# Kernel tuning notes

Measured on AMD Instinct MI355X. Metric: run time of the kernel, lower is better.

## Reference

```python
import jax, jax.numpy as jnp
import numpy as np

B, T, D, H = 512, 256, 64, 256


def setup_inputs() -> dict:
    key = jax.random.key(0)
    ks = jax.random.split(key, 12)
    X = jax.random.normal(ks[0], (B, T, D), dtype=jnp.float32)
    M = (jax.random.uniform(ks[1], (B, T, D)) < 0.7).astype(jnp.float32)
    # time since last observation, hours
    Delta = jax.random.uniform(ks[2], (B, T, D), dtype=jnp.float32) * 5.0
    x_mean = jax.random.normal(ks[3], (D,), dtype=jnp.float32) * 0.1
    s = 1.0 / np.sqrt(D)
    sh = 1.0 / np.sqrt(H)
    # input-decay Linear(D->D), hidden-decay Linear(D->H)
    W_gx = jax.random.uniform(ks[4], (D, D), minval=-s, maxval=s, dtype=jnp.float32)
    b_gx = jnp.zeros((D,), jnp.float32)
    W_gh = jax.random.uniform(ks[5], (D, H), minval=-s, maxval=s, dtype=jnp.float32)
    b_gh = jnp.zeros((H,), jnp.float32)
    # stacked gate weights for [z, r, h_tilde]
    W_x = jax.random.uniform(ks[6], (3, D, H), minval=-s, maxval=s, dtype=jnp.float32)
    W_h = jax.random.uniform(ks[7], (3, H, H), minval=-sh, maxval=sh, dtype=jnp.float32)
    W_m = jax.random.uniform(ks[8], (3, D, H), minval=-s, maxval=s, dtype=jnp.float32)
    b_g = jnp.zeros((3, H), jnp.float32)
    W_cls = jax.random.uniform(ks[9], (H, 1), minval=-sh, maxval=sh, dtype=jnp.float32)
    b_cls = jnp.zeros((1,), jnp.float32)
    return dict(X=X, M=M, Delta=Delta, x_mean=x_mean,
                W_gx=W_gx, b_gx=b_gx, W_gh=W_gh, b_gh=b_gh,
                W_x=W_x, W_h=W_h, W_m=W_m, b_g=b_g,
                W_cls=W_cls, b_cls=b_cls)


def reference(X, M, Delta, x_mean, W_gx, b_gx, W_gh, b_gh,
              W_x, W_h, W_m, b_g, W_cls, b_cls):
    Bn, Tn, Dn = X.shape
    Hn = W_h.shape[-1]

    def step(carry, inp):
        h, x_prev = carry          # [B,H], [B,D]
        x, m, d = inp              # each [B,D]
        gamma_x = jnp.exp(-jax.nn.relu(d @ W_gx + b_gx))   # [B,D]
        gamma_h = jnp.exp(-jax.nn.relu(d @ W_gh + b_gh))   # [B,H]
        # mean imputation with input decay
        x_hat = m * x + (1.0 - m) * (gamma_x * x_prev + (1.0 - gamma_x) * x_mean)
        hd = gamma_h * h                                   # hidden decay
        z = jax.nn.sigmoid(x_hat @ W_x[0] + hd @ W_h[0] + m @ W_m[0] + b_g[0])
        r = jax.nn.sigmoid(x_hat @ W_x[1] + hd @ W_h[1] + m @ W_m[1] + b_g[1])
        h_tilde = jnp.tanh(x_hat @ W_x[2] + (r * hd) @ W_h[2] + m @ W_m[2] + b_g[2])
        h_new = (1.0 - z) * hd + z * h_tilde
        x_prev_new = m * x + (1.0 - m) * x_prev            # carry last observation
        return (h_new, x_prev_new), None

    h0 = jnp.zeros((Bn, Hn), X.dtype)
    xp0 = jnp.zeros((Bn, Dn), X.dtype)
    xs = (jnp.swapaxes(X, 0, 1), jnp.swapaxes(M, 0, 1), jnp.swapaxes(Delta, 0, 1))
    (h, _), _ = jax.lax.scan(step, (h0, xp0), xs)
    return (h @ W_cls + b_cls)[:, 0]   # [B], classifier(h).squeeze(-1)
```

## Files before the change

kernel.cpp:

```cpp
#include <hip/hip_runtime.h>


constexpr int Bn = 512, Tn = 256, Dn = 64, Hn = 256;
constexpr int BB = 16, NBLK = Bn / BB;
constexpr int TC = 128;

typedef __attribute__((ext_vector_type(8))) short bf8_t;
typedef __attribute__((ext_vector_type(4))) float f4_t;

constexpr size_t OFF_WH  = 0;
constexpr size_t OFF_WX  = 196608;
constexpr size_t OFF_WM  = 245760;
constexpr size_t OFF_WGH = 294912;
constexpr size_t OFF_WGX = 311296;
constexpr int    PACK_SLOTS = 39424;

constexpr size_t GX_OFF  = (size_t)1 << 20;
constexpr size_t GH_OFF  = GX_OFF + (size_t)Bn * Tn * Dn * 4;
constexpr size_t WS_NEED = GH_OFF + (size_t)Bn * Tn * Hn * 2;

constexpr size_t GH2_OFF = (size_t)1 << 20;
constexpr size_t GX2_OFF = GH2_OFF + (size_t)Bn * Tn * Hn * 2;
constexpr size_t P2_OFF  = GX2_OFF;
constexpr size_t P2_SZ   = (size_t)3 * Bn * TC * Hn * 2;
constexpr size_t XH2_OFF = P2_OFF + P2_SZ;
constexpr size_t HST_OFF = XH2_OFF + (size_t)Bn * Tn * Dn * 2;
constexpr size_t WS_NEED3 = HST_OFF + (size_t)Bn * Hn * 2;

__device__ __forceinline__ unsigned short f2bf(float x) {
    union { float f; unsigned int u; } v; v.f = x;
    unsigned int r = (v.u + 0x7fffu + ((v.u >> 16) & 1u)) >> 16;
    return (unsigned short)r;
}
__device__ __forceinline__ float bf2f(unsigned short u) {
    union { unsigned int i; float f; } v; v.i = ((unsigned int)u) << 16; return v.f;
}
__device__ __forceinline__ bf8_t LD8(const short* p) { return *(const bf8_t*)p; }
__device__ __forceinline__ f4_t MF(bf8_t a, bf8_t b, f4_t c) {
    return __builtin_amdgcn_mfma_f32_16x16x32_bf16(a, b, c, 0, 0, 0);
}
__device__ __forceinline__ f4_t MFp(bf8_t a, const short* bp, f4_t c) {
    return MF(a, LD8(bp), c);
}
__device__ __forceinline__ const short* BA(const short* p, int ntG, int KT, int kt, int lane) {
    return p + (((size_t)ntG * KT + kt) * 64 + lane) * 8;
}
__device__ __forceinline__ void lds_sync() {
    __builtin_amdgcn_sched_barrier(0);
    asm volatile("s_waitcnt lgkmcnt(0)" ::: "memory");
    __builtin_amdgcn_s_barrier();
    __builtin_amdgcn_sched_barrier(0);
}

__global__ __launch_bounds__(256) void pack_weights(
    const float* __restrict__ W_gx, const float* __restrict__ W_gh,
    const float* __restrict__ W_x,  const float* __restrict__ W_h,
    const float* __restrict__ W_m,  short* __restrict__ out)
{
    const int slot = blockIdx.x * 256 + threadIdx.x;
    if (slot >= PACK_SLOTS) return;

    const float* w; int ldn, l, kt, j, kbase;
    if (slot < 24576) {
        int g = slot >> 13, rem = slot & 8191;
        int ntG = rem >> 9, r2 = rem & 511;
        kt = r2 >> 6; l = r2 & 63;
        j = ntG * 16 + (l & 15);
        w = W_h + (size_t)g * Hn * Hn; ldn = Hn;
    } else if (slot < 30720) {
        int s = slot - 24576;
        int g = s >> 11, rem = s & 2047;
        int ntG = rem >> 7, r2 = rem & 127;
        kt = r2 >> 6; l = r2 & 63;
        j = ntG * 16 + (l & 15);
        w = W_x + (size_t)g * Dn * Hn; ldn = Hn;
    } else if (slot < 36864) {
        int s = slot - 30720;
        int g = s >> 11, rem = s & 2047;
        int ntG = rem >> 7, r2 = rem & 127;
        kt = r2 >> 6; l = r2 & 63;
        j = ntG * 16 + (l & 15);
        w = W_m + (size_t)g * Dn * Hn; ldn = Hn;
    } else if (slot < 38912) {
        int s = slot - 36864;
        int ntG = s >> 7, r2 = s & 127;
        kt = r2 >> 6; l = r2 & 63;
        j = ntG * 16 + (l & 15);
        w = W_gh; ldn = Hn;
    } else {
        int s = slot - 38912;
        int ntG = s >> 7, r2 = s & 127;
        kt = r2 >> 6; l = r2 & 63;
        j = ntG * 16 + (l & 15);
        w = W_gx; ldn = Dn;
    }
    kbase = kt * 32 + ((l >> 4) << 3);
    bf8_t v;
    #pragma unroll
    for (int i = 0; i < 8; ++i)
        v[i] = (short)f2bf(w[(size_t)(kbase + i) * ldn + j]);
    *(bf8_t*)&out[(size_t)slot * 8] = v;
}

__global__ __launch_bounds__(256) void grud_prepass(
    const float* __restrict__ Dl, const float* __restrict__ b_gx,
    const float* __restrict__ b_gh, const short* __restrict__ pk,
    float* __restrict__ gx, unsigned short* __restrict__ gh)
{
    __shared__ short sDf[2 * 64 * 8];
    const int tid = threadIdx.x, w = tid >> 6, lane = tid & 63;
    const int bt = blockIdx.x >> 8, t = blockIdx.x & 255;
    const int b0 = bt * 16;
    const int c15 = lane & 15, rowb = (lane >> 4) * 4;

    if (w < 2) {
        const int row = lane & 15, cb = w * 32 + ((lane >> 4) << 3);
        const float* p = Dl + ((size_t)(b0 + row) * Tn + t) * Dn + cb;
        float4 a = *(const float4*)p, b = *(const float4*)(p + 4);
        bf8_t v;
        v[0]=(short)f2bf(a.x); v[1]=(short)f2bf(a.y); v[2]=(short)f2bf(a.z); v[3]=(short)f2bf(a.w);
        v[4]=(short)f2bf(b.x); v[5]=(short)f2bf(b.y); v[6]=(short)f2bf(b.z); v[7]=(short)f2bf(b.w);
        *(bf8_t*)&sDf[(w * 64 + lane) * 8] = v;
    }
    __syncthreads();
    bf8_t df0 = *(const bf8_t*)&sDf[lane * 8];
    bf8_t df1 = *(const bf8_t*)&sDf[(64 + lane) * 8];

    #pragma unroll
    for (int i = 0; i < 4; ++i) {
        const int ntG = 4 * w + i;
        f4_t acc = {0.f, 0.f, 0.f, 0.f};
        acc = MFp(df0, BA(pk + OFF_WGH, ntG, 2, 0, lane), acc);
        acc = MFp(df1, BA(pk + OFF_WGH, ntG, 2, 1, lane), acc);
        const int col = ntG * 16 + c15;
        const float bb = b_gh[col];
        #pragma unroll
        for (int q = 0; q < 4; ++q) {
            const int r = rowb + q;
            gh[((size_t)(b0 + r) * Tn + t) * Hn + col] =
                f2bf(__expf(-fmaxf(acc[q] + bb, 0.f)));
        }
    }
    {
        f4_t acc = {0.f, 0.f, 0.f, 0.f};
        acc = MFp(df0, BA(pk + OFF_WGX, w, 2, 0, lane), acc);
        acc = MFp(df1, BA(pk + OFF_WGX, w, 2, 1, lane), acc);
        const int col = w * 16 + c15;
        const float bb = b_gx[col];
        #pragma unroll
        for (int q = 0; q < 4; ++q) {
            const int r = rowb + q;
            gx[((size_t)(b0 + r) * Tn + t) * Dn + col] =
                __expf(-fmaxf(acc[q] + bb, 0.f));
        }
    }
}

__global__ __launch_bounds__(256) void grud_xhat(
    const float* __restrict__ X, const float* __restrict__ M,
    const float* __restrict__ x_mean, const float* __restrict__ gx,
    unsigned short* __restrict__ XH)
{
    const int g = blockIdx.x * 256 + threadIdx.x;
    const int b = g >> 6, d = g & 63;
    const float xm = x_mean[d];
    float xp = 0.f;
    const size_t base = (size_t)b * Tn * Dn + d;
    for (int t = 0; t < Tn; ++t) {
        const size_t idx = base + (size_t)t * Dn;
        const float x = X[idx], m = M[idx], gv = gx[idx];
        const float xh = m * x + (1.f - m) * (gv * xp + (1.f - gv) * xm);
        xp = m * x + (1.f - m) * xp;
        XH[idx] = f2bf(xh);
    }
}

__global__ __launch_bounds__(256) void grud_pgemm_c(
    const float* __restrict__ M, const unsigned short* __restrict__ XH,
    const float* __restrict__ b_g, const short* __restrict__ pk,
    unsigned short* __restrict__ P, int t0)
{
    const int tid = threadIdx.x, w = tid >> 6, lane = tid & 63;
    const int c15 = lane & 15;
    const int bblk = blockIdx.x >> 7;
    const int tl = blockIdx.x & (TC - 1);
    const int b0 = bblk * 16, t = t0 + tl;

    const size_t abase = ((size_t)(b0 + (lane & 15)) * Tn + t) * Dn + ((lane >> 4) << 3);
    bf8_t xf[2], mf[2];
    #pragma unroll
    for (int kt = 0; kt < 2; ++kt) {
        uint4 xa = *(const uint4*)&XH[abase + kt * 32];
        union { uint4 u; bf8_t b; } cvt; cvt.u = xa;
        xf[kt] = cvt.b;
        float4 a = *(const float4*)&M[abase + kt * 32];
        float4 b = *(const float4*)&M[abase + kt * 32 + 4];
        bf8_t v;
        v[0]=(short)f2bf(a.x); v[1]=(short)f2bf(a.y); v[2]=(short)f2bf(a.z); v[3]=(short)f2bf(a.w);
        v[4]=(short)f2bf(b.x); v[5]=(short)f2bf(b.y); v[6]=(short)f2bf(b.z); v[7]=(short)f2bf(b.w);
        mf[kt] = v;
    }

    const size_t btl = (size_t)blockIdx.x;
    #pragma unroll
    for (int i = 0; i < 12; ++i) {
        const int p = w * 12 + i;
        const int gg = p >> 4, ntG = p & 15;
        f4_t acc = {0.f, 0.f, 0.f, 0.f};
        acc = MFp(xf[0], BA(pk + OFF_WX + (size_t)gg * 16384, ntG, 2, 0, lane), acc);
        acc = MFp(xf[1], BA(pk + OFF_WX + (size_t)gg * 16384, ntG, 2, 1, lane), acc);
        acc = MFp(mf[0], BA(pk + OFF_WM + (size_t)gg * 16384, ntG, 2, 0, lane), acc);
        acc = MFp(mf[1], BA(pk + OFF_WM + (size_t)gg * 16384, ntG, 2, 1, lane), acc);
        const float bb = b_g[gg * Hn + ntG * 16 + c15];
        ushort4 o;
        o.x = f2bf(acc[0] + bb); o.y = f2bf(acc[1] + bb);
        o.z = f2bf(acc[2] + bb); o.w = f2bf(acc[3] + bb);
        *(ushort4*)&P[((btl * 3 + gg) * 16 + ntG) * 256 + lane * 4] = o;
    }
}

__global__ __launch_bounds__(512, 2) void grud_rec13(
    const float* __restrict__ W_cls, const float* __restrict__ b_cls,
    const short* __restrict__ pk, const unsigned short* __restrict__ gh,
    const unsigned short* __restrict__ P, unsigned short* __restrict__ hst,
    float* __restrict__ out, int t0, int lastc)
{
    __shared__ short sWh1[16 * 8 * 64 * 8];
    __shared__ unsigned short sh_hb[16][264];
    __shared__ short sA_hd[8 * 64 * 8];
    __shared__ short sA_rhd[8 * 64 * 8];

    const int tid = threadIdx.x, w = tid >> 6, lane = tid & 63;
    const int c15 = lane & 15, rowb = (lane >> 4) * 4;
    const int b0 = blockIdx.x * BB;
    unsigned short* hs = hst + (size_t)blockIdx.x * 16 * Hn;

    bf8_t whz[2][8], whh[2][8];
    #pragma unroll
    for (int nt = 0; nt < 2; ++nt)
        #pragma unroll
        for (int kt = 0; kt < 8; ++kt) {
            whz[nt][kt] = LD8(BA(pk + OFF_WH,             2 * w + nt, 8, kt, lane));
            whh[nt][kt] = LD8(BA(pk + OFF_WH + 2 * 65536, 2 * w + nt, 8, kt, lane));
        }
    for (int c = tid; c < 8192; c += 512)
        *(uint4*)&sWh1[c * 8] = *(const uint4*)&pk[OFF_WH + 65536 + (size_t)c * 8];

    float h_cd[2][4];
    if (t0 == 0) {
        for (int i = tid; i < 16 * 264; i += 512) (&sh_hb[0][0])[i] = 0;
        #pragma unroll
        for (int nt = 0; nt < 2; ++nt)
            #pragma unroll
            for (int q = 0; q < 4; ++q) h_cd[nt][q] = 0.f;
    } else {
        for (int i = tid; i < 16 * 256; i += 512)
            sh_hb[i >> 8][i & 255] = hs[i];
        #pragma unroll
        for (int nt = 0; nt < 2; ++nt)
            #pragma unroll
            for (int q = 0; q < 4; ++q)
                h_cd[nt][q] = bf2f(hs[(rowb + q) * Hn + w * 32 + nt * 16 + c15]);
    }

    const size_t ghA_base = ((size_t)(b0 + (lane & 15)) * Tn) * Hn + w * 32 + ((lane >> 4) << 3);
    uint4 gha = *(const uint4*)&gh[ghA_base + (size_t)t0 * Hn];
    unsigned short ghcd[2][4];
    #pragma unroll
    for (int nt = 0; nt < 2; ++nt)
        #pragma unroll
        for (int q = 0; q < 4; ++q)
            ghcd[nt][q] = gh[((size_t)(b0 + rowb + q) * Tn + t0) * Hn + w * 32 + nt * 16 + c15];

    ushort4 pz[2], pr[2], ph[2];
    {
        const size_t pbl = (size_t)blockIdx.x * TC;
        #pragma unroll
        for (int nt = 0; nt < 2; ++nt) {
            pz[nt] = *(const ushort4*)&P[((pbl * 3 + 0) * 16 + 2 * w + nt) * 256 + lane * 4];
            pr[nt] = *(const ushort4*)&P[((pbl * 3 + 1) * 16 + 2 * w + nt) * 256 + lane * 4];
            ph[nt] = *(const ushort4*)&P[((pbl * 3 + 2) * 16 + 2 * w + nt) * 256 + lane * 4];
        }
    }
    float hd_cd[2][4], zz[2][4];
    const f4_t z4 = {0.f, 0.f, 0.f, 0.f};
    __syncthreads();

    for (int tl = 0; tl < TC; ++tl) {
        const int tnl = (tl + 1 < TC) ? (tl + 1) : (TC - 1);
        const int tn  = t0 + tnl;

        {
            uint4 hA = *(const uint4*)&sh_hb[lane & 15][w * 32 + ((lane >> 4) << 3)];
            unsigned int ga[4] = {gha.x, gha.y, gha.z, gha.w};
            unsigned int ha[4] = {hA.x, hA.y, hA.z, hA.w};
            bf8_t hv;
            #pragma unroll
            for (int i = 0; i < 8; ++i) {
                float gf = bf2f((unsigned short)((ga[i >> 1] >> ((i & 1) * 16)) & 0xffffu));
                float hf = bf2f((unsigned short)((ha[i >> 1] >> ((i & 1) * 16)) & 0xffffu));
                hv[i] = (short)f2bf(gf * hf);
            }
            *(bf8_t*)&sA_hd[(w * 64 + lane) * 8] = hv;
        }
        #pragma unroll
        for (int nt = 0; nt < 2; ++nt)
            #pragma unroll
            for (int q = 0; q < 4; ++q)
                hd_cd[nt][q] = bf2f(ghcd[nt][q]) * h_cd[nt][q];

        uint4 gha_n = *(const uint4*)&gh[ghA_base + (size_t)tn * Hn];
        unsigned short ghcd_n[2][4];
        #pragma unroll
        for (int nt = 0; nt < 2; ++nt)
            #pragma unroll
            for (int q = 0; q < 4; ++q)
                ghcd_n[nt][q] = gh[((size_t)(b0 + rowb + q) * Tn + tn) * Hn + w * 32 + nt * 16 + c15];
        ushort4 pz_n[2], pr_n[2], ph_n[2];
        {
            const size_t pbl = (size_t)blockIdx.x * TC + tnl;
            #pragma unroll
            for (int nt = 0; nt < 2; ++nt) {
                pz_n[nt] = *(const ushort4*)&P[((pbl * 3 + 0) * 16 + 2 * w + nt) * 256 + lane * 4];
                pr_n[nt] = *(const ushort4*)&P[((pbl * 3 + 1) * 16 + 2 * w + nt) * 256 + lane * 4];
                ph_n[nt] = *(const ushort4*)&P[((pbl * 3 + 2) * 16 + 2 * w + nt) * 256 + lane * 4];
            }
        }
        lds_sync();

        f4_t aZ[2] = {z4, z4}, aR[2] = {z4, z4};
        #pragma unroll
        for (int kt = 0; kt < 8; ++kt) {
            bf8_t hf  = LD8(&sA_hd[(kt * 64 + lane) * 8]);
            bf8_t wr0 = LD8(&sWh1[((2 * w + 0) * 8 + kt) * 512 + lane * 8]);
            bf8_t wr1 = LD8(&sWh1[((2 * w + 1) * 8 + kt) * 512 + lane * 8]);
            aZ[0] = MF(hf, whz[0][kt], aZ[0]);
            aZ[1] = MF(hf, whz[1][kt], aZ[1]);
            aR[0] = MF(hf, wr0, aR[0]);
            aR[1] = MF(hf, wr1, aR[1]);
        }
        #pragma unroll
        for (int nt = 0; nt < 2; ++nt) {
            const int col = w * 32 + nt * 16 + c15;
            #pragma unroll
            for (int q = 0; q < 4; ++q) {
                const int r = rowb + q;
                float z  = 1.f / (1.f + __expf(-(aZ[nt][q] + bf2f(((const unsigned short*)&pz[nt])[q]))));
                float rr = 1.f / (1.f + __expf(-(aR[nt][q] + bf2f(((const unsigned short*)&pr[nt])[q]))));
                zz[nt][q] = z;
                sA_rhd[(w * 64 + ((col & 31) >> 3) * 16 + r) * 8 + (col & 7)] =
                    (short)f2bf(rr * hd_cd[nt][q]);
            }
        }
        lds_sync();

        f4_t aH[2] = {z4, z4};
        #pragma unroll
        for (int kt = 0; kt < 8; ++kt) {
            bf8_t rf = LD8(&sA_rhd[(kt * 64 + lane) * 8]);
            aH[0] = MF(rf, whh[0][kt], aH[0]);
            aH[1] = MF(rf, whh[1][kt], aH[1]);
        }
        #pragma unroll
        for (int nt = 0; nt < 2; ++nt) {
            const int col = w * 32 + nt * 16 + c15;
            #pragma unroll
            for (int q = 0; q < 4; ++q) {
                const int r = rowb + q;
                float pre = aH[nt][q] + bf2f(((const unsigned short*)&ph[nt])[q]);
                float a = fabsf(pre), e = __expf(-2.f * a);
                float th = copysignf((1.f - e) / (1.f + e), pre);
                float hn = (1.f - zz[nt][q]) * hd_cd[nt][q] + zz[nt][q] * th;
                h_cd[nt][q] = hn;
                sh_hb[r][col] = f2bf(hn);
            }
        }
        lds_sync();

        gha = gha_n;
        #pragma unroll
        for (int nt = 0; nt < 2; ++nt) {
            #pragma unroll
            for (int q = 0; q < 4; ++q) ghcd[nt][q] = ghcd_n[nt][q];
            pz[nt] = pz_n[nt]; pr[nt] = pr_n[nt]; ph[nt] = ph_n[nt];
        }
    }

    if (!lastc) {
        for (int i = tid; i < 16 * 256; i += 512)
            hs[i] = sh_hb[i >> 8][i & 255];
    } else {
        #pragma unroll
        for (int rr2 = 0; rr2 < 2; ++rr2) {
            const int row = w * 2 + rr2;
            ushort4 hb = *(const ushort4*)&sh_hb[row][lane * 4];
            float4 wv  = *(const float4*)&W_cls[lane * 4];
            float p = bf2f(hb.x) * wv.x + bf2f(hb.y) * wv.y +
                      bf2f(hb.z) * wv.z + bf2f(hb.w) * wv.w;
            #pragma unroll
            for (int o = 32; o > 0; o >>= 1) p += __shfl_down(p, o, 64);
            if (lane == 0) out[b0 + row] = p + b_cls[0];
        }
    }
}

__global__ __launch_bounds__(512, 2) void grud_rec8(
    const float* __restrict__ X, const float* __restrict__ M,
    const float* __restrict__ x_mean, const float* __restrict__ b_g,
    const float* __restrict__ W_cls, const float* __restrict__ b_cls,
    const short* __restrict__ pk, const float* __restrict__ gx,
    const unsigned short* __restrict__ gh, float* __restrict__ out)
{
    __shared__ short sWh1[16 * 8 * 64 * 8];
    __shared__ unsigned short sh_hb[16][264];
    __shared__ short sA_xh[2 * 64 * 8];
    __shared__ short sA_m [2 * 64 * 8];
    __shared__ short sA_hd[8 * 64 * 8];
    __shared__ short sA_rhd[8 * 64 * 8];

    const int tid = threadIdx.x, w = tid >> 6, lane = tid & 63;
    const int c15 = lane & 15, rowb = (lane >> 4) * 4;
    const int b0 = blockIdx.x * BB;

    bf8_t whz[2][8], whh[2][8];
    #pragma unroll
    for (int nt = 0; nt < 2; ++nt)
        #pragma unroll
        for (int kt = 0; kt < 8; ++kt) {
            whz[nt][kt] = LD8(BA(pk + OFF_WH,             2 * w + nt, 8, kt, lane));
            whh[nt][kt] = LD8(BA(pk + OFF_WH + 2 * 65536, 2 * w + nt, 8, kt, lane));
        }
    for (int c = tid; c < 8192; c += 512)
        *(uint4*)&sWh1[c * 8] = *(const uint4*)&pk[OFF_WH + 65536 + (size_t)c * 8];
    for (int i = tid; i < 16 * 264; i += 512) (&sh_hb[0][0])[i] = 0;

    const float bz[2] = { b_g[0 * Hn + w * 32 + c15], b_g[0 * Hn + w * 32 + 16 + c15] };
    const float brr[2]= { b_g[1 * Hn + w * 32 + c15], b_g[1 * Hn + w * 32 + 16 + c15] };
    const float bh[2] = { b_g[2 * Hn + w * 32 + c15], b_g[2 * Hn + w * 32 + 16 + c15] };

    const int s    = w * 32 + (lane & 31);
    const int kt2  = s >> 7, fl = (s >> 1) & 63, half = s & 1;
    const int brow = fl & 15, bcol = kt2 * 32 + ((fl >> 4) << 3) + half * 4;
    const size_t brow_base = ((size_t)(b0 + brow) * Tn) * Dn + bcol;

    float xb[4] = {0.f, 0.f, 0.f, 0.f};
    float xp[4] = {0.f, 0.f, 0.f, 0.f};
    float4 mv, xv = {0,0,0,0}, gxv = {0,0,0,0};
    if (lane < 32) {
        xb[0]=x_mean[bcol]; xb[1]=x_mean[bcol+1]; xb[2]=x_mean[bcol+2]; xb[3]=x_mean[bcol+3];
        xv  = *(const float4*)&X[brow_base];
        gxv = *(const float4*)&gx[brow_base];
    }
    mv = *(const float4*)&M[brow_base];

    const size_t ghA_base  = ((size_t)(b0 + (lane & 15)) * Tn) * Hn + w * 32 + ((lane >> 4) << 3);
    uint4 gha = *(const uint4*)&gh[ghA_base];
    unsigned short ghcd[2][4];
    #pragma unroll
    for (int nt = 0; nt < 2; ++nt)
        #pragma unroll
        for (int q = 0; q < 4; ++q)
            ghcd[nt][q] = gh[((size_t)(b0 + rowb + q) * Tn) * Hn + w * 32 + nt * 16 + c15];

    float h_cd[2][4] = {{0.f,0.f,0.f,0.f},{0.f,0.f,0.f,0.f}};
    float hd_cd[2][4], zz[2][4];
    const f4_t z4 = {0.f, 0.f, 0.f, 0.f};
    __syncthreads();

    for (int t = 0; t < Tn; ++t) {
        const int tn = (t + 1 < Tn) ? (t + 1) : (Tn - 1);

        {
            uint4 hA = *(const uint4*)&sh_hb[lane & 15][w * 32 + ((lane >> 4) << 3)];
            unsigned int ga[4] = {gha.x, gha.y, gha.z, gha.w};
            unsigned int ha[4] = {hA.x, hA.y, hA.z, hA.w};
            bf8_t hv;
            #pragma unroll
            for (int i = 0; i < 8; ++i) {
                float gf = bf2f((unsigned short)((ga[i >> 1] >> ((i & 1) * 16)) & 0xffffu));
                float hf = bf2f((unsigned short)((ha[i >> 1] >> ((i & 1) * 16)) & 0xffffu));
                hv[i] = (short)f2bf(gf * hf);
            }
            *(bf8_t*)&sA_hd[(w * 64 + lane) * 8] = hv;
        }
        #pragma unroll
        for (int nt = 0; nt < 2; ++nt)
            #pragma unroll
            for (int q = 0; q < 4; ++q)
                hd_cd[nt][q] = bf2f(ghcd[nt][q]) * h_cd[nt][q];

        if (lane < 32) {
            float mm[4] = {mv.x, mv.y, mv.z, mv.w};
            float xx[4] = {xv.x, xv.y, xv.z, xv.w};
            float gg[4] = {gxv.x, gxv.y, gxv.z, gxv.w};
            float xh[4];
            #pragma unroll
            for (int j = 0; j < 4; ++j) {
                xh[j] = mm[j] * xx[j] + (1.f - mm[j]) * (gg[j] * xp[j] + (1.f - gg[j]) * xb[j]);
                xp[j] = mm[j] * xx[j] + (1.f - mm[j]) * xp[j];
            }
            uint2 dd;
            dd.x = (unsigned int)f2bf(xh[0]) | ((unsigned int)f2bf(xh[1]) << 16);
            dd.y = (unsigned int)f2bf(xh[2]) | ((unsigned int)f2bf(xh[3]) << 16);
            *(uint2*)&sA_xh[(kt2 * 64 + fl) * 8 + half * 4] = dd;
        } else {
            uint2 dd;
            dd.x = (unsigned int)f2bf(mv.x) | ((unsigned int)f2bf(mv.y) << 16);
            dd.y = (unsigned int)f2bf(mv.z) | ((unsigned int)f2bf(mv.w) << 16);
            *(uint2*)&sA_m[(kt2 * 64 + fl) * 8 + half * 4] = dd;
        }
        {
            const size_t ba = brow_base + (size_t)tn * Dn;
            mv = *(const float4*)&M[ba];
            if (lane < 32) {
                xv  = *(const float4*)&X[ba];
                gxv = *(const float4*)&gx[ba];
            }
            gha = *(const uint4*)&gh[ghA_base + (size_t)tn * Hn];
            #pragma unroll
            for (int nt = 0; nt < 2; ++nt)
                #pragma unroll
                for (int q = 0; q < 4; ++q)
                    ghcd[nt][q] = gh[((size_t)(b0 + rowb + q) * Tn + tn) * Hn + w * 32 + nt * 16 + c15];
        }
        lds_sync();

        bf8_t wxz[2][2], wxr[2][2], wmz[2][2], wmr[2][2];
        #pragma unroll
        for (int nt = 0; nt < 2; ++nt)
            #pragma unroll
            for (int kt = 0; kt < 2; ++kt) {
                wxz[nt][kt] = LD8(BA(pk + OFF_WX,         2 * w + nt, 2, kt, lane));
                wxr[nt][kt] = LD8(BA(pk + OFF_WX + 16384, 2 * w + nt, 2, kt, lane));
                wmz[nt][kt] = LD8(BA(pk + OFF_WM,         2 * w + nt, 2, kt, lane));
                wmr[nt][kt] = LD8(BA(pk + OFF_WM + 16384, 2 * w + nt, 2, kt, lane));
            }
        bf8_t xf0 = LD8(&sA_xh[lane * 8]), xf1 = LD8(&sA_xh[(64 + lane) * 8]);
        bf8_t mf0 = LD8(&sA_m [lane * 8]), mf1 = LD8(&sA_m [(64 + lane) * 8]);

        f4_t aZ[2] = {z4, z4}, aR[2] = {z4, z4};
        #pragma unroll
        for (int kt = 0; kt < 8; ++kt) {
            bf8_t hf  = LD8(&sA_hd[(kt * 64 + lane) * 8]);
            bf8_t wr0 = LD8(&sWh1[((2 * w + 0) * 8 + kt) * 512 + lane * 8]);
            bf8_t wr1 = LD8(&sWh1[((2 * w + 1) * 8 + kt) * 512 + lane * 8]);
            aZ[0] = MF(hf, whz[0][kt], aZ[0]);
            aZ[1] = MF(hf, whz[1][kt], aZ[1]);
            aR[0] = MF(hf, wr0, aR[0]);
            aR[1] = MF(hf, wr1, aR[1]);
        }
        #pragma unroll
        for (int nt = 0; nt < 2; ++nt) {
            aZ[nt] = MF(xf0, wxz[nt][0], aZ[nt]); aZ[nt] = MF(xf1, wxz[nt][1], aZ[nt]);
            aZ[nt] = MF(mf0, wmz[nt][0], aZ[nt]); aZ[nt] = MF(mf1, wmz[nt][1], aZ[nt]);
            aR[nt] = MF(xf0, wxr[nt][0], aR[nt]); aR[nt] = MF(xf1, wxr[nt][1], aR[nt]);
            aR[nt] = MF(mf0, wmr[nt][0], aR[nt]); aR[nt] = MF(mf1, wmr[nt][1], aR[nt]);
        }
        bf8_t wxh[2][2], wmh[2][2];
        #pragma unroll
        for (int nt = 0; nt < 2; ++nt)
            #pragma unroll
            for (int kt = 0; kt < 2; ++kt) {
                wxh[nt][kt] = LD8(BA(pk + OFF_WX + 32768, 2 * w + nt, 2, kt, lane));
                wmh[nt][kt] = LD8(BA(pk + OFF_WM + 32768, 2 * w + nt, 2, kt, lane));
            }
        #pragma unroll
        for (int nt = 0; nt < 2; ++nt) {
            const int col = w * 32 + nt * 16 + c15;
            #pragma unroll
            for (int q = 0; q < 4; ++q) {
                const int r = rowb + q;
                float z  = 1.f / (1.f + __expf(-(aZ[nt][q] + bz[nt])));
                float rr = 1.f / (1.f + __expf(-(aR[nt][q] + brr[nt])));
                zz[nt][q] = z;
                sA_rhd[(w * 64 + ((col & 31) >> 3) * 16 + r) * 8 + (col & 7)] =
                    (short)f2bf(rr * hd_cd[nt][q]);
            }
        }
        lds_sync();

        f4_t aH[2] = {z4, z4};
        #pragma unroll
        for (int kt = 0; kt < 8; ++kt) {
            bf8_t rf = LD8(&sA_rhd[(kt * 64 + lane) * 8]);
            aH[0] = MF(rf, whh[0][kt], aH[0]);
            aH[1] = MF(rf, whh[1][kt], aH[1]);
        }
        #pragma unroll
        for (int nt = 0; nt < 2; ++nt) {
            aH[nt] = MF(xf0, wxh[nt][0], aH[nt]); aH[nt] = MF(xf1, wxh[nt][1], aH[nt]);
            aH[nt] = MF(mf0, wmh[nt][0], aH[nt]); aH[nt] = MF(mf1, wmh[nt][1], aH[nt]);
        }
        #pragma unroll
        for (int nt = 0; nt < 2; ++nt) {
            const int col = w * 32 + nt * 16 + c15;
            #pragma unroll
            for (int q = 0; q < 4; ++q) {
                const int r = rowb + q;
                float pre = aH[nt][q] + bh[nt];
                float a = fabsf(pre), e = __expf(-2.f * a);
                float th = copysignf((1.f - e) / (1.f + e), pre);
                float hn = (1.f - zz[nt][q]) * hd_cd[nt][q] + zz[nt][q] * th;
                h_cd[nt][q] = hn;
                sh_hb[r][col] = f2bf(hn);
            }
        }
        lds_sync();
    }

    #pragma unroll
    for (int rr2 = 0; rr2 < 2; ++rr2) {
        const int row = w * 2 + rr2;
        ushort4 hb = *(const ushort4*)&sh_hb[row][lane * 4];
        float4 wv  = *(const float4*)&W_cls[lane * 4];
        float p = bf2f(hb.x) * wv.x + bf2f(hb.y) * wv.y +
                  bf2f(hb.z) * wv.z + bf2f(hb.w) * wv.w;
        #pragma unroll
        for (int o = 32; o > 0; o >>= 1) p += __shfl_down(p, o, 64);
        if (lane == 0) out[b0 + row] = p + b_cls[0];
    }
}

extern "C" void kernel_launch(void* const* d_in, const int* in_sizes, int n_in,
                              void* d_out, int out_size, void* d_ws, size_t ws_size,
                              hipStream_t stream) {
    const float* X      = (const float*)d_in[0];
    const float* M      = (const float*)d_in[1];
    const float* Dl     = (const float*)d_in[2];
    const float* x_mean = (const float*)d_in[3];
    const float* W_gx   = (const float*)d_in[4];
    const float* b_gx   = (const float*)d_in[5];
    const float* W_gh   = (const float*)d_in[6];
    const float* b_gh   = (const float*)d_in[7];
    const float* W_x    = (const float*)d_in[8];
    const float* W_h    = (const float*)d_in[9];
    const float* W_m    = (const float*)d_in[10];
    const float* b_g    = (const float*)d_in[11];
    const float* W_cls  = (const float*)d_in[12];
    const float* b_cls  = (const float*)d_in[13];
    float* out = (float*)d_out;
    short* pk  = (short*)d_ws;

    hipLaunchKernelGGL(pack_weights, dim3((PACK_SLOTS + 255) / 256), dim3(256), 0, stream,
                       W_gx, W_gh, W_x, W_h, W_m, pk);

    if (ws_size >= WS_NEED3) {
        unsigned short* gh2 = (unsigned short*)((char*)d_ws + GH2_OFF);
        float*          gx2 = (float*)((char*)d_ws + GX2_OFF);
        unsigned short* P2  = (unsigned short*)((char*)d_ws + P2_OFF);
        unsigned short* xh2 = (unsigned short*)((char*)d_ws + XH2_OFF);
        unsigned short* hst = (unsigned short*)((char*)d_ws + HST_OFF);

        hipLaunchKernelGGL(grud_prepass, dim3(NBLK * Tn), dim3(256), 0, stream,
                           Dl, b_gx, b_gh, pk, gx2, gh2);
        hipLaunchKernelGGL(grud_xhat, dim3(Bn * Dn / 256), dim3(256), 0, stream,
                           X, M, x_mean, gx2, xh2);
        for (int c = 0; c < Tn / TC; ++c) {
            hipLaunchKernelGGL(grud_pgemm_c, dim3(NBLK * TC), dim3(256), 0, stream,
                               M, xh2, b_g, pk, P2, c * TC);
            hipLaunchKernelGGL(grud_rec13, dim3(NBLK), dim3(512), 0, stream,
                               W_cls, b_cls, pk, gh2, P2, hst, out,
                               c * TC, (c == Tn / TC - 1) ? 1 : 0);
        }
    } else {
        float*          gxbuf = (float*)((char*)d_ws + GX_OFF);
        unsigned short* ghbuf = (unsigned short*)((char*)d_ws + GH_OFF);
        hipLaunchKernelGGL(grud_prepass, dim3(NBLK * Tn), dim3(256), 0, stream,
                           Dl, b_gx, b_gh, pk, gxbuf, ghbuf);
        hipLaunchKernelGGL(grud_rec8, dim3(NBLK), dim3(512), 0, stream,
                           X, M, x_mean, b_g, W_cls, b_cls, pk, gxbuf, ghbuf, out);
    }
}
```

Before: 1.041 ms.

## Double recurrence block to 1024 threads, one 16-column tile per wave

The recurrent kernel now runs 16 waves per block instead of 8, with each wave owning a single 16-column output tile rather than two. This halves the per-wave MFMA chain and gate math on the serial per-timestep critical path, and halves the register-resident W_h fragments. In exchange there are more waves to join at each of the three per-step barriers, and half the waves sit idle during the hidden-decay staging. Only 32 blocks run, so the change is meant to raise parallelism inside each latency-bound block.

```diff
diff --git a/kernel.cpp b/kernel.cpp
--- a/kernel.cpp
+++ b/kernel.cpp
@@ -219,7 +219,7 @@
     }
 }
 
-__global__ __launch_bounds__(512, 2) void grud_rec13(
+__global__ __launch_bounds__(1024, 4) void grud_rec14(
     const float* __restrict__ W_cls, const float* __restrict__ b_cls,
     const short* __restrict__ pk, const unsigned short* __restrict__ gh,
     const unsigned short* __restrict__ P, unsigned short* __restrict__ hst,
@@ -233,56 +233,48 @@
     const int tid = threadIdx.x, w = tid >> 6, lane = tid & 63;
     const int c15 = lane & 15, rowb = (lane >> 4) * 4;
     const int b0 = blockIdx.x * BB;
+    const int col = w * 16 + c15;
     unsigned short* hs = hst + (size_t)blockIdx.x * 16 * Hn;
 
-    bf8_t whz[2][8], whh[2][8];
-    #pragma unroll
-    for (int nt = 0; nt < 2; ++nt)
-        #pragma unroll
-        for (int kt = 0; kt < 8; ++kt) {
-            whz[nt][kt] = LD8(BA(pk + OFF_WH,             2 * w + nt, 8, kt, lane));
-            whh[nt][kt] = LD8(BA(pk + OFF_WH + 2 * 65536, 2 * w + nt, 8, kt, lane));
-        }
-    for (int c = tid; c < 8192; c += 512)
+    bf8_t whz[8], whh[8];
+    #pragma unroll
+    for (int kt = 0; kt < 8; ++kt) {
+        whz[kt] = LD8(BA(pk + OFF_WH,             w, 8, kt, lane));
+        whh[kt] = LD8(BA(pk + OFF_WH + 2 * 65536, w, 8, kt, lane));
+    }
+    for (int c = tid; c < 8192; c += 1024)
         *(uint4*)&sWh1[c * 8] = *(const uint4*)&pk[OFF_WH + 65536 + (size_t)c * 8];
 
-    float h_cd[2][4];
+    float h_cd[4];
     if (t0 == 0) {
-        for (int i = tid; i < 16 * 264; i += 512) (&sh_hb[0][0])[i] = 0;
-        #pragma unroll
-        for (int nt = 0; nt < 2; ++nt)
-            #pragma unroll
-            for (int q = 0; q < 4; ++q) h_cd[nt][q] = 0.f;
+        for (int i = tid; i < 16 * 264; i += 1024) (&sh_hb[0][0])[i] = 0;
+        #pragma unroll
+        for (int q = 0; q < 4; ++q) h_cd[q] = 0.f;
     } else {
-        for (int i = tid; i < 16 * 256; i += 512)
+        for (int i = tid; i < 16 * 256; i += 1024)
             sh_hb[i >> 8][i & 255] = hs[i];
         #pragma unroll
-        for (int nt = 0; nt < 2; ++nt)
-            #pragma unroll
-            for (int q = 0; q < 4; ++q)
-                h_cd[nt][q] = bf2f(hs[(rowb + q) * Hn + w * 32 + nt * 16 + c15]);
-    }
-
-    const size_t ghA_base = ((size_t)(b0 + (lane & 15)) * Tn) * Hn + w * 32 + ((lane >> 4) << 3);
-    uint4 gha = *(const uint4*)&gh[ghA_base + (size_t)t0 * Hn];
-    unsigned short ghcd[2][4];
-    #pragma unroll
-    for (int nt = 0; nt < 2; ++nt)
-        #pragma unroll
         for (int q = 0; q < 4; ++q)
-            ghcd[nt][q] = gh[((size_t)(b0 + rowb + q) * Tn + t0) * Hn + w * 32 + nt * 16 + c15];
-
-    ushort4 pz[2], pr[2], ph[2];
+            h_cd[q] = bf2f(hs[(rowb + q) * Hn + col]);
+    }
+
+    const size_t ghA_base = ((size_t)(b0 + (lane & 15)) * Tn) * Hn
+                          + (w & 7) * 32 + ((lane >> 4) << 3);
+    uint4 gha = {0, 0, 0, 0};
+    if (w < 8) gha = *(const uint4*)&gh[ghA_base + (size_t)t0 * Hn];
+    unsigned short ghcd[4];
+    #pragma unroll
+    for (int q = 0; q < 4; ++q)
+        ghcd[q] = gh[((size_t)(b0 + rowb + q) * Tn + t0) * Hn + col];
+
+    ushort4 pz, pr, ph;
     {
         const size_t pbl = (size_t)blockIdx.x * TC;
-        #pragma unroll
-        for (int nt = 0; nt < 2; ++nt) {
-            pz[nt] = *(const ushort4*)&P[((pbl * 3 + 0) * 16 + 2 * w + nt) * 256 + lane * 4];
-            pr[nt] = *(const ushort4*)&P[((pbl * 3 + 1) * 16 + 2 * w + nt) * 256 + lane * 4];
-            ph[nt] = *(const ushort4*)&P[((pbl * 3 + 2) * 16 + 2 * w + nt) * 256 + lane * 4];
-        }
-    }
-    float hd_cd[2][4], zz[2][4];
+        pz = *(const ushort4*)&P[((pbl * 3 + 0) * 16 + w) * 256 + lane * 4];
+        pr = *(const ushort4*)&P[((pbl * 3 + 1) * 16 + w) * 256 + lane * 4];
+        ph = *(const ushort4*)&P[((pbl * 3 + 2) * 16 + w) * 256 + lane * 4];
+    }
+    float hd_cd[4], zz[4];
     const f4_t z4 = {0.f, 0.f, 0.f, 0.f};
     __syncthreads();
 
@@ -290,8 +282,8 @@
         const int tnl = (tl + 1 < TC) ? (tl + 1) : (TC - 1);
         const int tn  = t0 + tnl;
 
-        {
-            uint4 hA = *(const uint4*)&sh_hb[lane & 15][w * 32 + ((lane >> 4) << 3)];
+        if (w < 8) {
+            uint4 hA = *(const uint4*)&sh_hb[lane & 15][(w & 7) * 32 + ((lane >> 4) << 3)];
             unsigned int ga[4] = {gha.x, gha.y, gha.z, gha.w};
             unsigned int ha[4] = {hA.x, hA.y, hA.z, hA.w};
             bf8_t hv;
@@ -304,103 +296,78 @@
             *(bf8_t*)&sA_hd[(w * 64 + lane) * 8] = hv;
         }
         #pragma unroll
-        for (int nt = 0; nt < 2; ++nt)
-            #pragma unroll
-            for (int q = 0; q < 4; ++q)
-                hd_cd[nt][q] = bf2f(ghcd[nt][q]) * h_cd[nt][q];
-
-        uint4 gha_n = *(const uint4*)&gh[ghA_base + (size_t)tn * Hn];
-        unsigned short ghcd_n[2][4];
-        #pragma unroll
-        for (int nt = 0; nt < 2; ++nt)
-            #pragma unroll
-            for (int q = 0; q < 4; ++q)
-                ghcd_n[nt][q] = gh[((size_t)(b0 + rowb + q) * Tn + tn) * Hn + w * 32 + nt * 16 + c15];
-        ushort4 pz_n[2], pr_n[2], ph_n[2];
+        for (int q = 0; q < 4; ++q)
+            hd_cd[q] = bf2f(ghcd[q]) * h_cd[q];
+
+        uint4 gha_n = {0, 0, 0, 0};
+        if (w < 8) gha_n = *(const uint4*)&gh[ghA_base + (size_t)tn * Hn];
+        unsigned short ghcd_n[4];
+        #pragma unroll
+        for (int q = 0; q < 4; ++q)
+            ghcd_n[q] = gh[((size_t)(b0 + rowb + q) * Tn + tn) * Hn + col];
+        ushort4 pz_n, pr_n, ph_n;
         {
             const size_t pbl = (size_t)blockIdx.x * TC + tnl;
-            #pragma unroll
-            for (int nt = 0; nt < 2; ++nt) {
-                pz_n[nt] = *(const ushort4*)&P[((pbl * 3 + 0) * 16 + 2 * w + nt) * 256 + lane * 4];
-                pr_n[nt] = *(const ushort4*)&P[((pbl * 3 + 1) * 16 + 2 * w + nt) * 256 + lane * 4];
-                ph_n[nt] = *(const ushort4*)&P[((pbl * 3 + 2) * 16 + 2 * w + nt) * 256 + lane * 4];
-            }
+            pz_n = *(const ushort4*)&P[((pbl * 3 + 0) * 16 + w) * 256 + lane * 4];
+            pr_n = *(const ushort4*)&P[((pbl * 3 + 1) * 16 + w) * 256 + lane * 4];
+            ph_n = *(const ushort4*)&P[((pbl * 3 + 2) * 16 + w) * 256 + lane * 4];
         }
         lds_sync();
 
-        f4_t aZ[2] = {z4, z4}, aR[2] = {z4, z4};
+        f4_t aZ = z4, aR = z4;
         #pragma unroll
         for (int kt = 0; kt < 8; ++kt) {
-            bf8_t hf  = LD8(&sA_hd[(kt * 64 + lane) * 8]);
-            bf8_t wr0 = LD8(&sWh1[((2 * w + 0) * 8 + kt) * 512 + lane * 8]);
-            bf8_t wr1 = LD8(&sWh1[((2 * w + 1) * 8 + kt) * 512 + lane * 8]);
-            aZ[0] = MF(hf, whz[0][kt], aZ[0]);
-            aZ[1] = MF(hf, whz[1][kt], aZ[1]);
-            aR[0] = MF(hf, wr0, aR[0]);
-            aR[1] = MF(hf, wr1, aR[1]);
-        }
-        #pragma unroll
-        for (int nt = 0; nt < 2; ++nt) {
-            const int col = w * 32 + nt * 16 + c15;
-            #pragma unroll
-            for (int q = 0; q < 4; ++q) {
-                const int r = rowb + q;
-                float z  = 1.f / (1.f + __expf(-(aZ[nt][q] + bf2f(((const unsigned short*)&pz[nt])[q]))));
-                float rr = 1.f / (1.f + __expf(-(aR[nt][q] + bf2f(((const unsigned short*)&pr[nt])[q]))));
-                zz[nt][q] = z;
-                sA_rhd[(w * 64 + ((col & 31) >> 3) * 16 + r) * 8 + (col & 7)] =
-                    (short)f2bf(rr * hd_cd[nt][q]);
-            }
+            bf8_t hf = LD8(&sA_hd[(kt * 64 + lane) * 8]);
+            bf8_t wr = LD8(&sWh1[(w * 8 + kt) * 512 + lane * 8]);
+            aZ = MF(hf, whz[kt], aZ);
+            aR = MF(hf, wr, aR);
+        }
+        #pragma unroll
+        for (int q = 0; q < 4; ++q) {
+            const int r = rowb + q;
+            float z  = 1.f / (1.f + __expf(-(aZ[q] + bf2f(((const unsigned short*)&pz)[q]))));
+            float rr = 1.f / (1.f + __expf(-(aR[q] + bf2f(((const unsigned short*)&pr)[q]))));
+            zz[q] = z;
+            sA_rhd[((w >> 1) * 64 + ((col & 31) >> 3) * 16 + r) * 8 + (col & 7)] =
+                (short)f2bf(rr * hd_cd[q]);
         }
         lds_sync();
 
-        f4_t aH[2] = {z4, z4};
+        f4_t aH = z4;
         #pragma unroll
         for (int kt = 0; kt < 8; ++kt) {
             bf8_t rf = LD8(&sA_rhd[(kt * 64 + lane) * 8]);
-            aH[0] = MF(rf, whh[0][kt], aH[0]);
-            aH[1] = MF(rf, whh[1][kt], aH[1]);
-        }
-        #pragma unroll
-        for (int nt = 0; nt < 2; ++nt) {
-            const int col = w * 32 + nt * 16 + c15;
-            #pragma unroll
-            for (int q = 0; q < 4; ++q) {
-                const int r = rowb + q;
-                float pre = aH[nt][q] + bf2f(((const unsigned short*)&ph[nt])[q]);
-                float a = fabsf(pre), e = __expf(-2.f * a);
-                float th = copysignf((1.f - e) / (1.f + e), pre);
-                float hn = (1.f - zz[nt][q]) * hd_cd[nt][q] + zz[nt][q] * th;
-                h_cd[nt][q] = hn;
-                sh_hb[r][col] = f2bf(hn);
-            }
+            aH = MF(rf, whh[kt], aH);
+        }
+        #pragma unroll
+        for (int q = 0; q < 4; ++q) {
+            const int r = rowb + q;
+            float pre = aH[q] + bf2f(((const unsigned short*)&ph)[q]);
+            float a = fabsf(pre), e = __expf(-2.f * a);
+            float th = copysignf((1.f - e) / (1.f + e), pre);
+            float hn = (1.f - zz[q]) * hd_cd[q] + zz[q] * th;
+            h_cd[q] = hn;
+            sh_hb[r][col] = f2bf(hn);
         }
         lds_sync();
 
         gha = gha_n;
         #pragma unroll
-        for (int nt = 0; nt < 2; ++nt) {
-            #pragma unroll
-            for (int q = 0; q < 4; ++q) ghcd[nt][q] = ghcd_n[nt][q];
-            pz[nt] = pz_n[nt]; pr[nt] = pr_n[nt]; ph[nt] = ph_n[nt];
-        }
+        for (int q = 0; q < 4; ++q) ghcd[q] = ghcd_n[q];
+        pz = pz_n; pr = pr_n; ph = ph_n;
     }
 
     if (!lastc) {
-        for (int i = tid; i < 16 * 256; i += 512)
+        for (int i = tid; i < 16 * 256; i += 1024)
             hs[i] = sh_hb[i >> 8][i & 255];
     } else {
-        #pragma unroll
-        for (int rr2 = 0; rr2 < 2; ++rr2) {
-            const int row = w * 2 + rr2;
-            ushort4 hb = *(const ushort4*)&sh_hb[row][lane * 4];
-            float4 wv  = *(const float4*)&W_cls[lane * 4];
-            float p = bf2f(hb.x) * wv.x + bf2f(hb.y) * wv.y +
-                      bf2f(hb.z) * wv.z + bf2f(hb.w) * wv.w;
-            #pragma unroll
-            for (int o = 32; o > 0; o >>= 1) p += __shfl_down(p, o, 64);
-            if (lane == 0) out[b0 + row] = p + b_cls[0];
-        }
+        ushort4 hb = *(const ushort4*)&sh_hb[w][lane * 4];
+        float4 wv  = *(const float4*)&W_cls[lane * 4];
+        float p = bf2f(hb.x) * wv.x + bf2f(hb.y) * wv.y +
+                  bf2f(hb.z) * wv.z + bf2f(hb.w) * wv.w;
+        #pragma unroll
+        for (int o = 32; o > 0; o >>= 1) p += __shfl_down(p, o, 64);
+        if (lane == 0) out[b0 + w] = p + b_cls[0];
     }
 }
 
@@ -658,7 +625,7 @@
         for (int c = 0; c < Tn / TC; ++c) {
             hipLaunchKernelGGL(grud_pgemm_c, dim3(NBLK * TC), dim3(256), 0, stream,
                                M, xh2, b_g, pk, P2, c * TC);
-            hipLaunchKernelGGL(grud_rec13, dim3(NBLK), dim3(512), 0, stream,
+            hipLaunchKernelGGL(grud_rec14, dim3(NBLK), dim3(1024), 0, stream,
                                W_cls, b_cls, pk, gh2, P2, hst, out,
                                c * TC, (c == Tn / TC - 1) ? 1 : 0);
         }
```

After: 1.286 ms. 23.5% more time.
